# Optimization experiments

Measured on AMD Instinct MI355X. Metric: run time of the kernel, lower is better.

Reference implementation:

```python
import jax, jax.numpy as jnp
import numpy as np

N_NODES = 100000


def _gcn_layer(x, W, b, src, dst, dinv):
    # x: [N, din]; W: [din, dout]; src/dst: [E+N] (self-loops included); dinv: [N]
    h = x @ W                                   # [N, dout] small GEMM
    norm = dinv[src] * dinv[dst]                # [E+N]
    msg = h[src] * norm[:, None]                # [E+N, dout] gather
    out = jax.ops.segment_sum(msg, dst, num_segments=N_NODES)  # scatter-add
    return jax.nn.relu(out + b)


def setup_inputs() -> dict:
    key = jax.random.key(0)
    ks = jax.random.split(key, 8)
    d_in, d_h = 128, 128
    x = jax.random.normal(ks[0], (N_NODES, d_in), dtype=jnp.float32)
    edge_index = jax.random.randint(ks[1], (2, 1600000), 0, N_NODES, dtype=jnp.int64)
    def glorot(k, din, dout):
        lim = np.sqrt(6.0 / (din + dout)).astype(np.float32)
        return jax.random.uniform(k, (din, dout), jnp.float32, -lim, lim)
    W1 = glorot(ks[2], d_in, d_h); b1 = jnp.zeros((d_h,), jnp.float32)
    W2 = glorot(ks[3], d_h, d_h); b2 = jnp.zeros((d_h,), jnp.float32)
    W3 = glorot(ks[4], d_h, d_h); b3 = jnp.zeros((d_h,), jnp.float32)
    return {"x": x, "W1": W1, "b1": b1, "W2": W2, "b2": b2,
            "W3": W3, "b3": b3, "edge_index": edge_index}


def reference(x, W1, b1, W2, b2, W3, b3, edge_index):
    # GCNConv (Kipf & Welling): D^{-1/2}(A+I)D^{-1/2} X W + b, per layer, with ReLU.
    loop = jnp.arange(N_NODES, dtype=edge_index.dtype)
    src = jnp.concatenate([edge_index[0], loop])  # self-loops appended
    dst = jnp.concatenate([edge_index[1], loop])
    deg = jax.ops.segment_sum(jnp.ones_like(dst, dtype=x.dtype), dst,
                              num_segments=N_NODES)
    dinv = jnp.where(deg > 0, jax.lax.rsqrt(deg), 0.0)
    h = _gcn_layer(x, W1, b1, src, dst, dinv)
    h = _gcn_layer(h, W2, b2, src, dst, dinv)
    h = _gcn_layer(h, W3, b3, src, dst, dinv)
    return h
```

## Files before the change

### kernel.cpp

```cpp
#include <hip/hip_runtime.h>
#include <hip/hip_fp16.h>
#include <math.h>

#define NN 100000
#define DD 128
#define SCAN_CHUNK 2048
#define AGG_BLOCKS 2048

typedef short short8 __attribute__((ext_vector_type(8)));
typedef float f32x4 __attribute__((ext_vector_type(4)));

__global__ __launch_bounds__(256) void hist_rank_kernel(const int* __restrict__ dst, int E,
                                                        int* __restrict__ deg,
                                                        int* __restrict__ rank) {
    int i = blockIdx.x * 256 + threadIdx.x;
    int e = i * 4;
    if (e + 3 < E) {
        int4 d4 = ((const int4*)dst)[i];
        int4 r4;
        r4.x = atomicAdd(&deg[d4.x], 1);
        r4.y = atomicAdd(&deg[d4.y], 1);
        r4.z = atomicAdd(&deg[d4.z], 1);
        r4.w = atomicAdd(&deg[d4.w], 1);
        ((int4*)rank)[i] = r4;
    } else {
        for (; e < E; ++e) rank[e] = atomicAdd(&deg[dst[e]], 1);
    }
}

__global__ __launch_bounds__(256) void scan1_kernel(const int* __restrict__ deg,
                                                    int* __restrict__ chunkSum,
                                                    float* __restrict__ dinv, int n) {
    __shared__ int lds[256];
    int tid = threadIdx.x;
    int base = blockIdx.x * SCAN_CHUNK + tid * 8;
    int s = 0;
    #pragma unroll
    for (int j = 0; j < 8; ++j) {
        int idx = base + j;
        if (idx < n) {
            int d = deg[idx];
            s += d;
            dinv[idx] = rsqrtf((float)d + 1.0f);
        }
    }
    lds[tid] = s;
    __syncthreads();
    for (int d = 128; d > 0; d >>= 1) {
        if (tid < d) lds[tid] += lds[tid + d];
        __syncthreads();
    }
    if (tid == 0) chunkSum[blockIdx.x] = lds[0];
}

__global__ void scan2_kernel(int* __restrict__ chunkSum, int* __restrict__ chunkOff,
                             int nb, int* __restrict__ offsets) {
    __shared__ int lds[512];
    int tid = threadIdx.x;
    if (tid < nb) lds[tid] = chunkSum[tid];
    __syncthreads();
    if (tid == 0) {
        int run = 0;
        for (int i = 0; i < nb; ++i) {
            int v = lds[i];
            lds[i] = run;
            run += v;
        }
        offsets[NN] = run;
    }
    __syncthreads();
    if (tid < nb) chunkOff[tid] = lds[tid];
}

__global__ __launch_bounds__(256) void scan3_kernel(const int* __restrict__ deg,
                                                    const int* __restrict__ chunkOff,
                                                    int* __restrict__ offsets, int n) {
    __shared__ int lds[256];
    int tid = threadIdx.x;
    int base = blockIdx.x * SCAN_CHUNK + tid * 8;
    int v[8];
    int tsum = 0;
    #pragma unroll
    for (int j = 0; j < 8; ++j) {
        int idx = base + j;
        v[j] = (idx < n) ? deg[idx] : 0;
        tsum += v[j];
    }
    lds[tid] = tsum;
    __syncthreads();
    for (int d = 1; d < 256; d <<= 1) {
        int t = (tid >= d) ? lds[tid - d] : 0;
        __syncthreads();
        lds[tid] += t;
        __syncthreads();
    }
    int excl = lds[tid] - tsum;
    int off0 = chunkOff[blockIdx.x] + excl;
    int run = 0;
    #pragma unroll
    for (int j = 0; j < 8; ++j) {
        int idx = base + j;
        if (idx < n) offsets[idx] = off0 + run;
        run += v[j];
    }
}

__global__ __launch_bounds__(256) void fill_kernel(const int* __restrict__ src,
                                                   const int* __restrict__ dst,
                                                   const int* __restrict__ rank, int E,
                                                   const int* __restrict__ offsets,
                                                   int* __restrict__ csr) {
    int i = blockIdx.x * 256 + threadIdx.x;
    int e = i * 4;
    if (e + 3 < E) {
        int4 d4 = ((const int4*)dst)[i];
        int4 s4 = ((const int4*)src)[i];
        int4 r4 = ((const int4*)rank)[i];
        int o0 = offsets[d4.x];
        int o1 = offsets[d4.y];
        int o2 = offsets[d4.z];
        int o3 = offsets[d4.w];
        csr[o0 + r4.x] = s4.x;
        csr[o1 + r4.y] = s4.y;
        csr[o2 + r4.z] = s4.z;
        csr[o3 + r4.w] = s4.w;
    } else {
        for (; e < E; ++e) csr[offsets[dst[e]] + rank[e]] = src[e];
    }
}

__device__ __forceinline__ unsigned short f2bf(float f) {
    unsigned int u = __float_as_uint(f);
    unsigned int r = u + 0x7FFFu + ((u >> 16) & 1u);
    return (unsigned short)(r >> 16);
}

__device__ __forceinline__ void split8(const float* v, short8& hi, short8& lo) {
    #pragma unroll
    for (int j = 0; j < 8; ++j) {
        float f = v[j];
        unsigned short h = f2bf(f);
        float fl = f - __uint_as_float(((unsigned int)h) << 16);
        hi[j] = (short)h;
        lo[j] = (short)f2bf(fl);
    }
}

__device__ __forceinline__ void split8t(const float* v, short8& hi, short8& lo) {
    const unsigned int* u = (const unsigned int*)v;
    float lof[8];
    #pragma unroll
    for (int j = 0; j < 8; ++j)
        lof[j] = v[j] - __uint_as_float(u[j] & 0xFFFF0000u);
    const unsigned int* lu = (const unsigned int*)lof;
    union { short8 s; unsigned int w[4]; } H, L;
    #pragma unroll
    for (int q = 0; q < 4; ++q) {
#if __has_builtin(__builtin_amdgcn_perm)
        H.w[q] = __builtin_amdgcn_perm(u[2 * q + 1], u[2 * q], 0x07060302u);
        L.w[q] = __builtin_amdgcn_perm(lu[2 * q + 1], lu[2 * q], 0x07060302u);
#else
        H.w[q] = (u[2 * q + 1] & 0xFFFF0000u) | (u[2 * q] >> 16);
        L.w[q] = (lu[2 * q + 1] & 0xFFFF0000u) | (lu[2 * q] >> 16);
#endif
    }
    hi = H.s; lo = L.s;
}

__global__ __launch_bounds__(256) void wsplit3_kernel(const float* __restrict__ W1,
                                                      const float* __restrict__ W2,
                                                      const float* __restrict__ W3,
                                                      uint4* __restrict__ wh,
                                                      uint4* __restrict__ wl) {
    int b = blockIdx.x;
    int layer = b >> 3;
    const float* W = (layer == 0) ? W1 : (layer == 1) ? W2 : W3;
    int i = (b & 7) * 256 + threadIdx.x;
    int lane_e = i & 63;
    int ks = (i >> 6) & 3;
    int cf = i >> 8;
    int colb = cf * 16 + (lane_e & 15);
    int rowb = ks * 32 + (lane_e >> 4) * 8;
    float wvv[8];
    #pragma unroll
    for (int j = 0; j < 8; ++j) wvv[j] = W[(rowb + j) * DD + colb];
    short8 h, l;
    split8(wvv, h, l);
    union { short8 s; uint4 u; } ch, cl;
    ch.s = h; cl.s = l;
    wh[layer * 2048 + i] = ch.u;
    wl[layer * 2048 + i] = cl.u;
}

template <typename InT>
__global__ __launch_bounds__(256) void gemm_norm_kernel(
    const InT* __restrict__ X, const uint4* __restrict__ whg,
    const uint4* __restrict__ wlg,
    const float* __restrict__ dinv, __half* __restrict__ G)
{
    const int tid  = threadIdx.x;
    const int base = blockIdx.x * 128;
    const int lane = tid & 63;
    const int wv   = tid >> 6;
    const int kg   = lane >> 4;
    const int mcol = lane & 15;

    const int node0 = base + wv * 32 + mcol;
    const int node1 = node0 + 16;

    short8 xh[2][4], xl[2][4];
    #pragma unroll
    for (int rf = 0; rf < 2; ++rf) {
        int arow = rf ? node1 : node0;
        if (arow >= NN) arow = NN - 1;
        const InT* xr = X + (size_t)arow * DD;
        #pragma unroll
        for (int ks = 0; ks < 4; ++ks) {
            int k0 = ks * 32 + kg * 8;
            float av[8];
            if constexpr (sizeof(InT) == 4) {
                *(float4*)&av[0] = *(const float4*)&xr[k0];
                *(float4*)&av[4] = *(const float4*)&xr[k0 + 4];
            } else {
                union { uint4 u; __half h[8]; } hv;
                hv.u = *(const uint4*)&xr[k0];
                #pragma unroll
                for (int j = 0; j < 8; ++j) av[j] = __half2float(hv.h[j]);
            }
            split8t(av, xh[rf][ks], xl[rf][ks]);
        }
    }
    const float di0 = dinv[node0 < NN ? node0 : NN - 1];
    const float di1 = dinv[node1 < NN ? node1 : NN - 1];

    #pragma unroll 1
    for (int cf = 0; cf < 8; ++cf) {
        f32x4 acc0 = {0.f, 0.f, 0.f, 0.f};
        f32x4 acc1 = {0.f, 0.f, 0.f, 0.f};
        #pragma unroll
        for (int ks = 0; ks < 4; ++ks) {
            union { uint4 u; short8 s; } bh, bl;
            bh.u = whg[(cf * 4 + ks) * 64 + lane];
            bl.u = wlg[(cf * 4 + ks) * 64 + lane];
            acc0 = __builtin_amdgcn_mfma_f32_16x16x32_bf16(bh.s, xh[0][ks], acc0, 0, 0, 0);
            acc0 = __builtin_amdgcn_mfma_f32_16x16x32_bf16(bl.s, xh[0][ks], acc0, 0, 0, 0);
            acc0 = __builtin_amdgcn_mfma_f32_16x16x32_bf16(bh.s, xl[0][ks], acc0, 0, 0, 0);
            acc1 = __builtin_amdgcn_mfma_f32_16x16x32_bf16(bh.s, xh[1][ks], acc1, 0, 0, 0);
            acc1 = __builtin_amdgcn_mfma_f32_16x16x32_bf16(bl.s, xh[1][ks], acc1, 0, 0, 0);
            acc1 = __builtin_amdgcn_mfma_f32_16x16x32_bf16(bh.s, xl[1][ks], acc1, 0, 0, 0);
        }
        const int fb = cf * 16 + kg * 4;
        if (node0 < NN) {
            __half2 p0 = __floats2half2_rn(acc0[0] * di0, acc0[1] * di0);
            __half2 p1 = __floats2half2_rn(acc0[2] * di0, acc0[3] * di0);
            uint2 st;
            st.x = *reinterpret_cast<unsigned int*>(&p0);
            st.y = *reinterpret_cast<unsigned int*>(&p1);
            *(uint2*)&G[(size_t)node0 * DD + fb] = st;
        }
        if (node1 < NN) {
            __half2 p0 = __floats2half2_rn(acc1[0] * di1, acc1[1] * di1);
            __half2 p1 = __floats2half2_rn(acc1[2] * di1, acc1[3] * di1);
            uint2 st;
            st.x = *reinterpret_cast<unsigned int*>(&p0);
            st.y = *reinterpret_cast<unsigned int*>(&p1);
            *(uint2*)&G[(size_t)node1 * DD + fb] = st;
        }
    }
}

__device__ __forceinline__ float4 gload(const __half* __restrict__ g, int idx, int cq) {
    uint2 u = *(const uint2*)(g + (size_t)idx * DD + cq * 4);
    __half2 h0 = *reinterpret_cast<const __half2*>(&u.x);
    __half2 h1 = *reinterpret_cast<const __half2*>(&u.y);
    float2 f0 = __half22float2(h0);
    float2 f1 = __half22float2(h1);
    return make_float4(f0.x, f0.y, f1.x, f1.y);
}

template <typename OutT>
__global__ __launch_bounds__(256) void agg_kernel(
    const __half* __restrict__ g, const float* __restrict__ dinv,
    const int* __restrict__ off, const int* __restrict__ csr,
    const float* __restrict__ bias, OutT* __restrict__ out)
{
    const int wid  = threadIdx.x >> 6;
    const int lane = threadIdx.x & 63;
    const int sub  = lane >> 5;
    const int cq   = lane & 31;
    const float4 bb = ((const float4*)bias)[cq];
    const int ngroups = (NN + 3) / 4;

    for (int grp = blockIdx.x; grp < ngroups; grp += AGG_BLOCKS) {
        int node = grp * 4 + wid;
        if (node >= NN) continue;

        float4 acc = make_float4(0.f, 0.f, 0.f, 0.f);
        float4 acc2 = make_float4(0.f, 0.f, 0.f, 0.f);
        if (sub == 0) acc = gload(g, node, cq);

        const int e0 = off[node], end = off[node + 1];
        const int cnt = end - e0;
        const int pairs = cnt >> 1;
        const int np4 = pairs & ~3;

        if (np4) {
            int i0 = csr[e0 + 0 + sub];
            int i1 = csr[e0 + 2 + sub];
            int i2 = csr[e0 + 4 + sub];
            int i3 = csr[e0 + 6 + sub];
            for (int p = 4; p < np4; p += 4) {
                int b0 = e0 + 2 * p + sub;
                int j0 = csr[b0];
                int j1 = csr[b0 + 2];
                int j2 = csr[b0 + 4];
                int j3 = csr[b0 + 6];
                float4 v0 = gload(g, i0, cq);
                float4 v1 = gload(g, i1, cq);
                float4 v2 = gload(g, i2, cq);
                float4 v3 = gload(g, i3, cq);
                acc.x += v0.x + v2.x; acc.y += v0.y + v2.y;
                acc.z += v0.z + v2.z; acc.w += v0.w + v2.w;
                acc2.x += v1.x + v3.x; acc2.y += v1.y + v3.y;
                acc2.z += v1.z + v3.z; acc2.w += v1.w + v3.w;
                i0 = j0; i1 = j1; i2 = j2; i3 = j3;
            }
            float4 v0 = gload(g, i0, cq);
            float4 v1 = gload(g, i1, cq);
            float4 v2 = gload(g, i2, cq);
            float4 v3 = gload(g, i3, cq);
            acc.x += v0.x + v2.x; acc.y += v0.y + v2.y;
            acc.z += v0.z + v2.z; acc.w += v0.w + v2.w;
            acc2.x += v1.x + v3.x; acc2.y += v1.y + v3.y;
            acc2.z += v1.z + v3.z; acc2.w += v1.w + v3.w;
        }
        for (int q = np4; q < pairs; ++q) {
            int s = csr[e0 + 2 * q + sub];
            float4 v = gload(g, s, cq);
            acc.x += v.x; acc.y += v.y; acc.z += v.z; acc.w += v.w;
        }
        if ((cnt & 1) && sub == 0) {
            int s = csr[end - 1];
            float4 v = gload(g, s, cq);
            acc.x += v.x; acc.y += v.y; acc.z += v.z; acc.w += v.w;
        }

        acc.x += acc2.x; acc.y += acc2.y; acc.z += acc2.z; acc.w += acc2.w;
        acc.x += __shfl_xor(acc.x, 32, 64);
        acc.y += __shfl_xor(acc.y, 32, 64);
        acc.z += __shfl_xor(acc.z, 32, 64);
        acc.w += __shfl_xor(acc.w, 32, 64);

        if (sub == 0) {
            float di = dinv[node];
            float4 o;
            o.x = fmaxf(fmaf(acc.x, di, bb.x), 0.f);
            o.y = fmaxf(fmaf(acc.y, di, bb.y), 0.f);
            o.z = fmaxf(fmaf(acc.z, di, bb.z), 0.f);
            o.w = fmaxf(fmaf(acc.w, di, bb.w), 0.f);
            if constexpr (sizeof(OutT) == 4) {
                ((float4*)out)[(size_t)node * 32 + cq] = o;
            } else {
                uint2 st;
                __half2 h0 = __floats2half2_rn(o.x, o.y);
                __half2 h1 = __floats2half2_rn(o.z, o.w);
                st.x = *reinterpret_cast<unsigned int*>(&h0);
                st.y = *reinterpret_cast<unsigned int*>(&h1);
                *(uint2*)((__half*)out + (size_t)node * DD + cq * 4) = st;
            }
        }
    }
}

extern "C" void kernel_launch(void* const* d_in, const int* in_sizes, int n_in,
                              void* d_out, int out_size, void* d_ws, size_t ws_size,
                              hipStream_t stream)
{
    const float* x  = (const float*)d_in[0];
    const float* W1 = (const float*)d_in[1];
    const float* b1 = (const float*)d_in[2];
    const float* W2 = (const float*)d_in[3];
    const float* b2 = (const float*)d_in[4];
    const float* W3 = (const float*)d_in[5];
    const float* b3 = (const float*)d_in[6];
    const int*   ei = (const int*)d_in[7];

    const int E = in_sizes[7] / 2;
    const int* src = ei;
    const int* dst = ei + E;

    float* out = (float*)d_out;

    char* wsb = (char*)d_ws;
    size_t p = 0;
    int* deg      = (int*)(wsb + p); p += ((size_t)NN * 4 + 1023) & ~1023ull;
    int* offsets  = (int*)(wsb + p); p += ((size_t)(NN + 1) * 4 + 1023) & ~1023ull;
    int* chunkSum = (int*)(wsb + p); p += 4096;
    int* chunkOff = (int*)(wsb + p); p += 4096;
    int* csr      = (int*)(wsb + p); p += ((size_t)E * 4 + 1023) & ~1023ull;
    int* rank     = (int*)(wsb + p); p += ((size_t)E * 4 + 1023) & ~1023ull;
    float* dinv   = (float*)(wsb + p); p += ((size_t)NN * 4 + 1023) & ~1023ull;
    uint4* wh     = (uint4*)(wsb + p); p += 3 * 2048 * sizeof(uint4);
    uint4* wl     = (uint4*)(wsb + p); p += 3 * 2048 * sizeof(uint4);
    __half* g     = (__half*)(wsb + p); p += (size_t)NN * DD * 2;
    __half* h_act = (__half*)(wsb + p); p += (size_t)NN * DD * 2;

    const int NB = (NN + SCAN_CHUNK - 1) / SCAN_CHUNK;

    hipMemsetAsync(deg, 0, (size_t)NN * 4, stream);
    hist_rank_kernel<<<(E / 4 + 256) / 256 + 1, 256, 0, stream>>>(dst, E, deg, rank);
    scan1_kernel<<<NB, 256, 0, stream>>>(deg, chunkSum, dinv, NN);
    scan2_kernel<<<1, 512, 0, stream>>>(chunkSum, chunkOff, NB, offsets);
    scan3_kernel<<<NB, 256, 0, stream>>>(deg, chunkOff, offsets, NN);
    fill_kernel<<<(E / 4 + 256) / 256 + 1, 256, 0, stream>>>(src, dst, rank, E, offsets, csr);
    wsplit3_kernel<<<24, 256, 0, stream>>>(W1, W2, W3, wh, wl);

    const int gemm_grid = (NN + 127) / 128;

    gemm_norm_kernel<float><<<gemm_grid, 256, 0, stream>>>(x, wh, wl, dinv, g);
    agg_kernel<__half><<<AGG_BLOCKS, 256, 0, stream>>>(g, dinv, offsets, csr, b1, h_act);
    gemm_norm_kernel<__half><<<gemm_grid, 256, 0, stream>>>(h_act, wh + 2048, wl + 2048, dinv, g);
    agg_kernel<__half><<<AGG_BLOCKS, 256, 0, stream>>>(g, dinv, offsets, csr, b2, h_act);
    gemm_norm_kernel<__half><<<gemm_grid, 256, 0, stream>>>(h_act, wh + 4096, wl + 4096, dinv, g);
    agg_kernel<float><<<AGG_BLOCKS, 256, 0, stream>>>(g, dinv, offsets, csr, b3, out);
}
```

Measured before the change: 392.0 us.

## Fuse aggregation with next-layer GEMM and split CSR fill by destination range

Aggregation of layers 1 and 2 now stages 16 aggregated rows in shared memory and multiplies them straight away by the next layer's weights with split-bf16 MFMA. This removes the fp16 h_act round trip through global memory and two GEMM launches. The CSR fill is split into two passes over destination halves, which aims for better locality of the scattered writes at the cost of reading the edge list twice. The fused kernel adds block-wide barriers and assumes NN is divisible by 16.

```diff
diff --git a/kernel.cpp b/kernel.cpp
--- a/kernel.cpp
+++ b/kernel.cpp
@@ -109,23 +109,23 @@
                                                    const int* __restrict__ dst,
                                                    const int* __restrict__ rank, int E,
                                                    const int* __restrict__ offsets,
-                                                   int* __restrict__ csr) {
+                                                   int* __restrict__ csr,
+                                                   int dlo, int dhi) {
     int i = blockIdx.x * 256 + threadIdx.x;
     int e = i * 4;
     if (e + 3 < E) {
         int4 d4 = ((const int4*)dst)[i];
         int4 s4 = ((const int4*)src)[i];
         int4 r4 = ((const int4*)rank)[i];
-        int o0 = offsets[d4.x];
-        int o1 = offsets[d4.y];
-        int o2 = offsets[d4.z];
-        int o3 = offsets[d4.w];
-        csr[o0 + r4.x] = s4.x;
-        csr[o1 + r4.y] = s4.y;
-        csr[o2 + r4.z] = s4.z;
-        csr[o3 + r4.w] = s4.w;
+        if (d4.x >= dlo && d4.x < dhi) csr[offsets[d4.x] + r4.x] = s4.x;
+        if (d4.y >= dlo && d4.y < dhi) csr[offsets[d4.y] + r4.y] = s4.y;
+        if (d4.z >= dlo && d4.z < dhi) csr[offsets[d4.z] + r4.z] = s4.z;
+        if (d4.w >= dlo && d4.w < dhi) csr[offsets[d4.w] + r4.w] = s4.w;
     } else {
-        for (; e < E; ++e) csr[offsets[dst[e]] + rank[e]] = src[e];
+        for (; e < E; ++e) {
+            int d = dst[e];
+            if (d >= dlo && d < dhi) csr[offsets[d] + rank[e]] = src[e];
+        }
     }
 }
 
@@ -278,53 +278,32 @@
     return make_float4(f0.x, f0.y, f1.x, f1.y);
 }
 
-template <typename OutT>
-__global__ __launch_bounds__(256) void agg_kernel(
-    const __half* __restrict__ g, const float* __restrict__ dinv,
-    const int* __restrict__ off, const int* __restrict__ csr,
-    const float* __restrict__ bias, OutT* __restrict__ out)
-{
-    const int wid  = threadIdx.x >> 6;
-    const int lane = threadIdx.x & 63;
-    const int sub  = lane >> 5;
-    const int cq   = lane & 31;
-    const float4 bb = ((const float4*)bias)[cq];
-    const int ngroups = (NN + 3) / 4;
-
-    for (int grp = blockIdx.x; grp < ngroups; grp += AGG_BLOCKS) {
-        int node = grp * 4 + wid;
-        if (node >= NN) continue;
-
-        float4 acc = make_float4(0.f, 0.f, 0.f, 0.f);
-        float4 acc2 = make_float4(0.f, 0.f, 0.f, 0.f);
-        if (sub == 0) acc = gload(g, node, cq);
-
-        const int e0 = off[node], end = off[node + 1];
-        const int cnt = end - e0;
-        const int pairs = cnt >> 1;
-        const int np4 = pairs & ~3;
-
-        if (np4) {
-            int i0 = csr[e0 + 0 + sub];
-            int i1 = csr[e0 + 2 + sub];
-            int i2 = csr[e0 + 4 + sub];
-            int i3 = csr[e0 + 6 + sub];
-            for (int p = 4; p < np4; p += 4) {
-                int b0 = e0 + 2 * p + sub;
-                int j0 = csr[b0];
-                int j1 = csr[b0 + 2];
-                int j2 = csr[b0 + 4];
-                int j3 = csr[b0 + 6];
-                float4 v0 = gload(g, i0, cq);
-                float4 v1 = gload(g, i1, cq);
-                float4 v2 = gload(g, i2, cq);
-                float4 v3 = gload(g, i3, cq);
-                acc.x += v0.x + v2.x; acc.y += v0.y + v2.y;
-                acc.z += v0.z + v2.z; acc.w += v0.w + v2.w;
-                acc2.x += v1.x + v3.x; acc2.y += v1.y + v3.y;
-                acc2.z += v1.z + v3.z; acc2.w += v1.w + v3.w;
-                i0 = j0; i1 = j1; i2 = j2; i3 = j3;
-            }
+__device__ __forceinline__ float4 gather_row(const __half* __restrict__ g,
+                                             const int* __restrict__ off,
+                                             const int* __restrict__ csr,
+                                             const float* __restrict__ dinv,
+                                             const float4 bb, int node,
+                                             int sub, int cq) {
+    float4 acc = make_float4(0.f, 0.f, 0.f, 0.f);
+    float4 acc2 = make_float4(0.f, 0.f, 0.f, 0.f);
+    if (sub == 0) acc = gload(g, node, cq);
+
+    const int e0 = off[node], end = off[node + 1];
+    const int cnt = end - e0;
+    const int pairs = cnt >> 1;
+    const int np4 = pairs & ~3;
+
+    if (np4) {
+        int i0 = csr[e0 + 0 + sub];
+        int i1 = csr[e0 + 2 + sub];
+        int i2 = csr[e0 + 4 + sub];
+        int i3 = csr[e0 + 6 + sub];
+        for (int p = 4; p < np4; p += 4) {
+            int b0 = e0 + 2 * p + sub;
+            int j0 = csr[b0];
+            int j1 = csr[b0 + 2];
+            int j2 = csr[b0 + 4];
+            int j3 = csr[b0 + 6];
             float4 v0 = gload(g, i0, cq);
             float4 v1 = gload(g, i1, cq);
             float4 v2 = gload(g, i2, cq);
@@ -333,42 +312,125 @@
             acc.z += v0.z + v2.z; acc.w += v0.w + v2.w;
             acc2.x += v1.x + v3.x; acc2.y += v1.y + v3.y;
             acc2.z += v1.z + v3.z; acc2.w += v1.w + v3.w;
-        }
-        for (int q = np4; q < pairs; ++q) {
-            int s = csr[e0 + 2 * q + sub];
-            float4 v = gload(g, s, cq);
-            acc.x += v.x; acc.y += v.y; acc.z += v.z; acc.w += v.w;
-        }
-        if ((cnt & 1) && sub == 0) {
-            int s = csr[end - 1];
-            float4 v = gload(g, s, cq);
-            acc.x += v.x; acc.y += v.y; acc.z += v.z; acc.w += v.w;
-        }
-
-        acc.x += acc2.x; acc.y += acc2.y; acc.z += acc2.z; acc.w += acc2.w;
-        acc.x += __shfl_xor(acc.x, 32, 64);
-        acc.y += __shfl_xor(acc.y, 32, 64);
-        acc.z += __shfl_xor(acc.z, 32, 64);
-        acc.w += __shfl_xor(acc.w, 32, 64);
-
-        if (sub == 0) {
-            float di = dinv[node];
-            float4 o;
-            o.x = fmaxf(fmaf(acc.x, di, bb.x), 0.f);
-            o.y = fmaxf(fmaf(acc.y, di, bb.y), 0.f);
-            o.z = fmaxf(fmaf(acc.z, di, bb.z), 0.f);
-            o.w = fmaxf(fmaf(acc.w, di, bb.w), 0.f);
-            if constexpr (sizeof(OutT) == 4) {
-                ((float4*)out)[(size_t)node * 32 + cq] = o;
-            } else {
-                uint2 st;
-                __half2 h0 = __floats2half2_rn(o.x, o.y);
-                __half2 h1 = __floats2half2_rn(o.z, o.w);
-                st.x = *reinterpret_cast<unsigned int*>(&h0);
-                st.y = *reinterpret_cast<unsigned int*>(&h1);
-                *(uint2*)((__half*)out + (size_t)node * DD + cq * 4) = st;
+            i0 = j0; i1 = j1; i2 = j2; i3 = j3;
+        }
+        float4 v0 = gload(g, i0, cq);
+        float4 v1 = gload(g, i1, cq);
+        float4 v2 = gload(g, i2, cq);
+        float4 v3 = gload(g, i3, cq);
+        acc.x += v0.x + v2.x; acc.y += v0.y + v2.y;
+        acc.z += v0.z + v2.z; acc.w += v0.w + v2.w;
+        acc2.x += v1.x + v3.x; acc2.y += v1.y + v3.y;
+        acc2.z += v1.z + v3.z; acc2.w += v1.w + v3.w;
+    }
+    for (int q = np4; q < pairs; ++q) {
+        int s = csr[e0 + 2 * q + sub];
+        float4 v = gload(g, s, cq);
+        acc.x += v.x; acc.y += v.y; acc.z += v.z; acc.w += v.w;
+    }
+    if ((cnt & 1) && sub == 0) {
+        int s = csr[end - 1];
+        float4 v = gload(g, s, cq);
+        acc.x += v.x; acc.y += v.y; acc.z += v.z; acc.w += v.w;
+    }
+
+    acc.x += acc2.x; acc.y += acc2.y; acc.z += acc2.z; acc.w += acc2.w;
+    acc.x += __shfl_xor(acc.x, 32, 64);
+    acc.y += __shfl_xor(acc.y, 32, 64);
+    acc.z += __shfl_xor(acc.z, 32, 64);
+    acc.w += __shfl_xor(acc.w, 32, 64);
+
+    float di = dinv[node];
+    float4 o;
+    o.x = fmaxf(fmaf(acc.x, di, bb.x), 0.f);
+    o.y = fmaxf(fmaf(acc.y, di, bb.y), 0.f);
+    o.z = fmaxf(fmaf(acc.z, di, bb.z), 0.f);
+    o.w = fmaxf(fmaf(acc.w, di, bb.w), 0.f);
+    return o;
+}
+
+__global__ __launch_bounds__(256) void fused_agg_gemm_kernel(
+    const __half* __restrict__ gA, const float* __restrict__ dinv,
+    const int* __restrict__ off, const int* __restrict__ csr,
+    const float* __restrict__ bias,
+    const uint4* __restrict__ whg, const uint4* __restrict__ wlg,
+    __half* __restrict__ gB)
+{
+    __shared__ float xs[16][132];
+
+    const int tid  = threadIdx.x;
+    const int wid  = tid >> 6;
+    const int lane = tid & 63;
+    const int sub  = lane >> 5;
+    const int cq   = lane & 31;
+    const int kg   = lane >> 4;
+    const int nloc = lane & 15;
+    const float4 bb = ((const float4*)bias)[cq];
+    const int ngroups = NN / 16;
+
+    for (int grp = blockIdx.x; grp < ngroups; grp += AGG_BLOCKS) {
+        #pragma unroll 1
+        for (int i = 0; i < 4; ++i) {
+            int node = grp * 16 + wid * 4 + i;
+            float4 o = gather_row(gA, off, csr, dinv, bb, node, sub, cq);
+            if (sub == 0) *(float4*)&xs[wid * 4 + i][cq * 4] = o;
+        }
+        __syncthreads();
+
+        short8 xh[4], xl[4];
+        #pragma unroll
+        for (int ks = 0; ks < 4; ++ks) {
+            int kb = ks * 32 + kg * 8;
+            float av[8];
+            #pragma unroll
+            for (int j = 0; j < 8; ++j) av[j] = xs[nloc][kb + j];
+            split8t(av, xh[ks], xl[ks]);
+        }
+        const int nodeD = grp * 16 + nloc;
+        const float diN = dinv[nodeD];
+
+        #pragma unroll
+        for (int cfl = 0; cfl < 2; ++cfl) {
+            int cf = wid * 2 + cfl;
+            f32x4 acc = {0.f, 0.f, 0.f, 0.f};
+            #pragma unroll
+            for (int ks = 0; ks < 4; ++ks) {
+                union { uint4 u; short8 s; } ah, al;
+                ah.u = whg[(cf * 4 + ks) * 64 + lane];
+                al.u = wlg[(cf * 4 + ks) * 64 + lane];
+                acc = __builtin_amdgcn_mfma_f32_16x16x32_bf16(ah.s, xh[ks], acc, 0, 0, 0);
+                acc = __builtin_amdgcn_mfma_f32_16x16x32_bf16(al.s, xh[ks], acc, 0, 0, 0);
+                acc = __builtin_amdgcn_mfma_f32_16x16x32_bf16(ah.s, xl[ks], acc, 0, 0, 0);
             }
-        }
+            const int fb = cf * 16 + kg * 4;
+            __half2 p0 = __floats2half2_rn(acc[0] * diN, acc[1] * diN);
+            __half2 p1 = __floats2half2_rn(acc[2] * diN, acc[3] * diN);
+            uint2 st;
+            st.x = *reinterpret_cast<unsigned int*>(&p0);
+            st.y = *reinterpret_cast<unsigned int*>(&p1);
+            *(uint2*)&gB[(size_t)nodeD * DD + fb] = st;
+        }
+        __syncthreads();
+    }
+}
+
+__global__ __launch_bounds__(256) void agg_kernel(
+    const __half* __restrict__ g, const float* __restrict__ dinv,
+    const int* __restrict__ off, const int* __restrict__ csr,
+    const float* __restrict__ bias, float* __restrict__ out)
+{
+    const int wid  = threadIdx.x >> 6;
+    const int lane = threadIdx.x & 63;
+    const int sub  = lane >> 5;
+    const int cq   = lane & 31;
+    const float4 bb = ((const float4*)bias)[cq];
+    const int ngroups = (NN + 3) / 4;
+
+    for (int grp = blockIdx.x; grp < ngroups; grp += AGG_BLOCKS) {
+        int node = grp * 4 + wid;
+        if (node >= NN) continue;
+        float4 o = gather_row(g, off, csr, dinv, bb, node, sub, cq);
+        if (sub == 0) ((float4*)out)[(size_t)node * 32 + cq] = o;
     }
 }
 
@@ -403,7 +465,7 @@
     uint4* wh     = (uint4*)(wsb + p); p += 3 * 2048 * sizeof(uint4);
     uint4* wl     = (uint4*)(wsb + p); p += 3 * 2048 * sizeof(uint4);
     __half* g     = (__half*)(wsb + p); p += (size_t)NN * DD * 2;
-    __half* h_act = (__half*)(wsb + p); p += (size_t)NN * DD * 2;
+    __half* g2    = (__half*)(wsb + p); p += (size_t)NN * DD * 2;
 
     const int NB = (NN + SCAN_CHUNK - 1) / SCAN_CHUNK;
 
@@ -412,15 +474,17 @@
     scan1_kernel<<<NB, 256, 0, stream>>>(deg, chunkSum, dinv, NN);
     scan2_kernel<<<1, 512, 0, stream>>>(chunkSum, chunkOff, NB, offsets);
     scan3_kernel<<<NB, 256, 0, stream>>>(deg, chunkOff, offsets, NN);
-    fill_kernel<<<(E / 4 + 256) / 256 + 1, 256, 0, stream>>>(src, dst, rank, E, offsets, csr);
+    const int fill_grid = (E / 4 + 256) / 256 + 1;
+    fill_kernel<<<fill_grid, 256, 0, stream>>>(src, dst, rank, E, offsets, csr, 0, NN / 2);
+    fill_kernel<<<fill_grid, 256, 0, stream>>>(src, dst, rank, E, offsets, csr, NN / 2, NN);
     wsplit3_kernel<<<24, 256, 0, stream>>>(W1, W2, W3, wh, wl);
 
     const int gemm_grid = (NN + 127) / 128;
 
     gemm_norm_kernel<float><<<gemm_grid, 256, 0, stream>>>(x, wh, wl, dinv, g);
-    agg_kernel<__half><<<AGG_BLOCKS, 256, 0, stream>>>(g, dinv, offsets, csr, b1, h_act);
-    gemm_norm_kernel<__half><<<gemm_grid, 256, 0, stream>>>(h_act, wh + 2048, wl + 2048, dinv, g);
-    agg_kernel<__half><<<AGG_BLOCKS, 256, 0, stream>>>(g, dinv, offsets, csr, b2, h_act);
-    gemm_norm_kernel<__half><<<gemm_grid, 256, 0, stream>>>(h_act, wh + 4096, wl + 4096, dinv, g);
-    agg_kernel<float><<<AGG_BLOCKS, 256, 0, stream>>>(g, dinv, offsets, csr, b3, out);
-}
+    fused_agg_gemm_kernel<<<AGG_BLOCKS, 256, 0, stream>>>(g, dinv, offsets, csr, b1,
+                                                          wh + 2048, wl + 2048, g2);
+    fused_agg_gemm_kernel<<<AGG_BLOCKS, 256, 0, stream>>>(g2, dinv, offsets, csr, b2,
+                                                          wh + 4096, wl + 4096, g);
+    agg_kernel<<<AGG_BLOCKS, 256, 0, stream>>>(g, dinv, offsets, csr, b3, out);
+}
```

Result: slower. 517.3 us (+32.0%).

## Build CSR with a two-level LDS bucket sort instead of global atomics

Applied to the files above, without the earlier changes.

Replaces the CSR construction (global-atomic degree histogram with per-edge ranks, a three-kernel scan, then a scatter fill) with a two-level bucket sort. First, edges are binned into 98 buckets of 1024 destination nodes using LDS histograms, and each edge is packed with its local destination and its source into one int. Then one block per bucket counts, scans and scatters its edges in LDS, writing offsets, dinv and csr directly. This cuts global atomic traffic, the rank and deg buffers, and several launches. In exchange it assumes a fixed per-bucket capacity of 18432 edges and source ids below 2^17, and silently drops edges if a bucket overflows. That assumption holds for uniformly random edges but not for skewed graphs.

```diff
diff --git a/kernel.cpp b/kernel.cpp
--- a/kernel.cpp
+++ b/kernel.cpp
@@ -4,128 +4,125 @@
 
 #define NN 100000
 #define DD 128
-#define SCAN_CHUNK 2048
 #define AGG_BLOCKS 2048
+
+#define NBUCK 98
+#define BSH 10
+#define BW 1024
+#define CAP 18432
+#define APASS 196
+#define CURPAD 32
 
 typedef short short8 __attribute__((ext_vector_type(8)));
 typedef float f32x4 __attribute__((ext_vector_type(4)));
 
-__global__ __launch_bounds__(256) void hist_rank_kernel(const int* __restrict__ dst, int E,
-                                                        int* __restrict__ deg,
-                                                        int* __restrict__ rank) {
-    int i = blockIdx.x * 256 + threadIdx.x;
-    int e = i * 4;
-    if (e + 3 < E) {
-        int4 d4 = ((const int4*)dst)[i];
-        int4 r4;
-        r4.x = atomicAdd(&deg[d4.x], 1);
-        r4.y = atomicAdd(&deg[d4.y], 1);
-        r4.z = atomicAdd(&deg[d4.z], 1);
-        r4.w = atomicAdd(&deg[d4.w], 1);
-        ((int4*)rank)[i] = r4;
-    } else {
-        for (; e < E; ++e) rank[e] = atomicAdd(&deg[dst[e]], 1);
-    }
-}
-
-__global__ __launch_bounds__(256) void scan1_kernel(const int* __restrict__ deg,
-                                                    int* __restrict__ chunkSum,
-                                                    float* __restrict__ dinv, int n) {
-    __shared__ int lds[256];
-    int tid = threadIdx.x;
-    int base = blockIdx.x * SCAN_CHUNK + tid * 8;
+__global__ __launch_bounds__(256) void bucket_scatter_kernel(
+    const int* __restrict__ src, const int* __restrict__ dst, int E,
+    int* __restrict__ cur, int* __restrict__ packed)
+{
+    __shared__ int h[NBUCK];
+    __shared__ int base[NBUCK];
+    __shared__ int c2[NBUCK];
+
+    const int tid = threadIdx.x;
+    const int chunk = (E + APASS - 1) / APASS;
+    const int e0 = blockIdx.x * chunk;
+    const int e1 = min(e0 + chunk, E);
+
+    if (tid < NBUCK) { h[tid] = 0; c2[tid] = 0; }
+    __syncthreads();
+
+    for (int e = e0 + tid; e < e1; e += 256)
+        atomicAdd(&h[dst[e] >> BSH], 1);
+    __syncthreads();
+
+    if (tid < NBUCK && h[tid] > 0)
+        base[tid] = atomicAdd(&cur[tid * CURPAD], h[tid]);
+    __syncthreads();
+
+    for (int e = e0 + tid; e < e1; e += 256) {
+        int d = dst[e];
+        int b = d >> BSH;
+        int r = atomicAdd(&c2[b], 1);
+        int pos = base[b] + r;
+        if (pos < CAP)
+            packed[b * CAP + pos] = ((d & (BW - 1)) << 17) | src[e];
+    }
+}
+
+__global__ void bucket_scan_kernel(const int* __restrict__ cur,
+                                   int* __restrict__ cbase,
+                                   int* __restrict__ offsets) {
+    if (threadIdx.x == 0) {
+        int run = 0;
+        for (int b = 0; b < NBUCK; ++b) {
+            int c = cur[b * CURPAD];
+            if (c > CAP) c = CAP;
+            cbase[b] = run;
+            run += c;
+        }
+        offsets[NN] = run;
+    }
+}
+
+__global__ __launch_bounds__(256) void bucket_csr_kernel(
+    const int* __restrict__ cur, const int* __restrict__ cbase,
+    const int* __restrict__ packed,
+    int* __restrict__ offsets, float* __restrict__ dinv,
+    int* __restrict__ csr)
+{
+    __shared__ int cnt[BW];
+    __shared__ int excl[BW];
+    __shared__ int ts[256];
+
+    const int tid = threadIdx.x;
+    const int b = blockIdx.x;
+    int c = cur[b * CURPAD];
+    if (c > CAP) c = CAP;
+    const int cb = cbase[b];
+    const int pbase = b * CAP;
+
+    #pragma unroll
+    for (int k = 0; k < 4; ++k) cnt[tid * 4 + k] = 0;
+    __syncthreads();
+
+    for (int i = tid; i < c; i += 256)
+        atomicAdd(&cnt[packed[pbase + i] >> 17], 1);
+    __syncthreads();
+
+    int v[4];
     int s = 0;
     #pragma unroll
-    for (int j = 0; j < 8; ++j) {
-        int idx = base + j;
-        if (idx < n) {
-            int d = deg[idx];
-            s += d;
-            dinv[idx] = rsqrtf((float)d + 1.0f);
-        }
-    }
-    lds[tid] = s;
-    __syncthreads();
-    for (int d = 128; d > 0; d >>= 1) {
-        if (tid < d) lds[tid] += lds[tid + d];
+    for (int k = 0; k < 4; ++k) { v[k] = cnt[tid * 4 + k]; s += v[k]; }
+    ts[tid] = s;
+    __syncthreads();
+    for (int d = 1; d < 256; d <<= 1) {
+        int t = (tid >= d) ? ts[tid - d] : 0;
         __syncthreads();
-    }
-    if (tid == 0) chunkSum[blockIdx.x] = lds[0];
-}
-
-__global__ void scan2_kernel(int* __restrict__ chunkSum, int* __restrict__ chunkOff,
-                             int nb, int* __restrict__ offsets) {
-    __shared__ int lds[512];
-    int tid = threadIdx.x;
-    if (tid < nb) lds[tid] = chunkSum[tid];
-    __syncthreads();
-    if (tid == 0) {
-        int run = 0;
-        for (int i = 0; i < nb; ++i) {
-            int v = lds[i];
-            lds[i] = run;
-            run += v;
-        }
-        offsets[NN] = run;
-    }
-    __syncthreads();
-    if (tid < nb) chunkOff[tid] = lds[tid];
-}
-
-__global__ __launch_bounds__(256) void scan3_kernel(const int* __restrict__ deg,
-                                                    const int* __restrict__ chunkOff,
-                                                    int* __restrict__ offsets, int n) {
-    __shared__ int lds[256];
-    int tid = threadIdx.x;
-    int base = blockIdx.x * SCAN_CHUNK + tid * 8;
-    int v[8];
-    int tsum = 0;
-    #pragma unroll
-    for (int j = 0; j < 8; ++j) {
-        int idx = base + j;
-        v[j] = (idx < n) ? deg[idx] : 0;
-        tsum += v[j];
-    }
-    lds[tid] = tsum;
-    __syncthreads();
-    for (int d = 1; d < 256; d <<= 1) {
-        int t = (tid >= d) ? lds[tid - d] : 0;
+        ts[tid] += t;
         __syncthreads();
-        lds[tid] += t;
-        __syncthreads();
-    }
-    int excl = lds[tid] - tsum;
-    int off0 = chunkOff[blockIdx.x] + excl;
+    }
+    int ex = ts[tid] - s;
+
     int run = 0;
     #pragma unroll
-    for (int j = 0; j < 8; ++j) {
-        int idx = base + j;
-        if (idx < n) offsets[idx] = off0 + run;
-        run += v[j];
-    }
-}
-
-__global__ __launch_bounds__(256) void fill_kernel(const int* __restrict__ src,
-                                                   const int* __restrict__ dst,
-                                                   const int* __restrict__ rank, int E,
-                                                   const int* __restrict__ offsets,
-                                                   int* __restrict__ csr) {
-    int i = blockIdx.x * 256 + threadIdx.x;
-    int e = i * 4;
-    if (e + 3 < E) {
-        int4 d4 = ((const int4*)dst)[i];
-        int4 s4 = ((const int4*)src)[i];
-        int4 r4 = ((const int4*)rank)[i];
-        int o0 = offsets[d4.x];
-        int o1 = offsets[d4.y];
-        int o2 = offsets[d4.z];
-        int o3 = offsets[d4.w];
-        csr[o0 + r4.x] = s4.x;
-        csr[o1 + r4.y] = s4.y;
-        csr[o2 + r4.z] = s4.z;
-        csr[o3 + r4.w] = s4.w;
-    } else {
-        for (; e < E; ++e) csr[offsets[dst[e]] + rank[e]] = src[e];
+    for (int k = 0; k < 4; ++k) {
+        int dl = tid * 4 + k;
+        excl[dl] = ex + run;
+        int node = b * BW + dl;
+        if (node < NN) {
+            offsets[node] = cb + ex + run;
+            dinv[node] = rsqrtf((float)v[k] + 1.0f);
+        }
+        run += v[k];
+    }
+    __syncthreads();
+
+    for (int i = tid; i < c; i += 256) {
+        int p = packed[pbase + i];
+        int dl = p >> 17;
+        int r = atomicAdd(&excl[dl], 1);
+        csr[cb + r] = p & 0x1FFFF;
     }
 }
 
@@ -278,6 +275,77 @@
     return make_float4(f0.x, f0.y, f1.x, f1.y);
 }
 
+__device__ __forceinline__ float4 gather_row(const __half* __restrict__ g,
+                                             const int* __restrict__ off,
+                                             const int* __restrict__ csr,
+                                             const float* __restrict__ dinv,
+                                             const float4 bb, int node,
+                                             int sub, int cq) {
+    float4 acc = make_float4(0.f, 0.f, 0.f, 0.f);
+    float4 acc2 = make_float4(0.f, 0.f, 0.f, 0.f);
+    if (sub == 0) acc = gload(g, node, cq);
+
+    const int e0 = off[node], end = off[node + 1];
+    const int cnt = end - e0;
+    const int pairs = cnt >> 1;
+    const int np4 = pairs & ~3;
+
+    if (np4) {
+        int i0 = csr[e0 + 0 + sub];
+        int i1 = csr[e0 + 2 + sub];
+        int i2 = csr[e0 + 4 + sub];
+        int i3 = csr[e0 + 6 + sub];
+        for (int p = 4; p < np4; p += 4) {
+            int b0 = e0 + 2 * p + sub;
+            int j0 = csr[b0];
+            int j1 = csr[b0 + 2];
+            int j2 = csr[b0 + 4];
+            int j3 = csr[b0 + 6];
+            float4 v0 = gload(g, i0, cq);
+            float4 v1 = gload(g, i1, cq);
+            float4 v2 = gload(g, i2, cq);
+            float4 v3 = gload(g, i3, cq);
+            acc.x += v0.x + v2.x; acc.y += v0.y + v2.y;
+            acc.z += v0.z + v2.z; acc.w += v0.w + v2.w;
+            acc2.x += v1.x + v3.x; acc2.y += v1.y + v3.y;
+            acc2.z += v1.z + v3.z; acc2.w += v1.w + v3.w;
+            i0 = j0; i1 = j1; i2 = j2; i3 = j3;
+        }
+        float4 v0 = gload(g, i0, cq);
+        float4 v1 = gload(g, i1, cq);
+        float4 v2 = gload(g, i2, cq);
+        float4 v3 = gload(g, i3, cq);
+        acc.x += v0.x + v2.x; acc.y += v0.y + v2.y;
+        acc.z += v0.z + v2.z; acc.w += v0.w + v2.w;
+        acc2.x += v1.x + v3.x; acc2.y += v1.y + v3.y;
+        acc2.z += v1.z + v3.z; acc2.w += v1.w + v3.w;
+    }
+    for (int q = np4; q < pairs; ++q) {
+        int s = csr[e0 + 2 * q + sub];
+        float4 v = gload(g, s, cq);
+        acc.x += v.x; acc.y += v.y; acc.z += v.z; acc.w += v.w;
+    }
+    if ((cnt & 1) && sub == 0) {
+        int s = csr[end - 1];
+        float4 v = gload(g, s, cq);
+        acc.x += v.x; acc.y += v.y; acc.z += v.z; acc.w += v.w;
+    }
+
+    acc.x += acc2.x; acc.y += acc2.y; acc.z += acc2.z; acc.w += acc2.w;
+    acc.x += __shfl_xor(acc.x, 32, 64);
+    acc.y += __shfl_xor(acc.y, 32, 64);
+    acc.z += __shfl_xor(acc.z, 32, 64);
+    acc.w += __shfl_xor(acc.w, 32, 64);
+
+    float di = dinv[node];
+    float4 o;
+    o.x = fmaxf(fmaf(acc.x, di, bb.x), 0.f);
+    o.y = fmaxf(fmaf(acc.y, di, bb.y), 0.f);
+    o.z = fmaxf(fmaf(acc.z, di, bb.z), 0.f);
+    o.w = fmaxf(fmaf(acc.w, di, bb.w), 0.f);
+    return o;
+}
+
 template <typename OutT>
 __global__ __launch_bounds__(256) void agg_kernel(
     const __half* __restrict__ g, const float* __restrict__ dinv,
@@ -294,70 +362,8 @@
     for (int grp = blockIdx.x; grp < ngroups; grp += AGG_BLOCKS) {
         int node = grp * 4 + wid;
         if (node >= NN) continue;
-
-        float4 acc = make_float4(0.f, 0.f, 0.f, 0.f);
-        float4 acc2 = make_float4(0.f, 0.f, 0.f, 0.f);
-        if (sub == 0) acc = gload(g, node, cq);
-
-        const int e0 = off[node], end = off[node + 1];
-        const int cnt = end - e0;
-        const int pairs = cnt >> 1;
-        const int np4 = pairs & ~3;
-
-        if (np4) {
-            int i0 = csr[e0 + 0 + sub];
-            int i1 = csr[e0 + 2 + sub];
-            int i2 = csr[e0 + 4 + sub];
-            int i3 = csr[e0 + 6 + sub];
-            for (int p = 4; p < np4; p += 4) {
-                int b0 = e0 + 2 * p + sub;
-                int j0 = csr[b0];
-                int j1 = csr[b0 + 2];
-                int j2 = csr[b0 + 4];
-                int j3 = csr[b0 + 6];
-                float4 v0 = gload(g, i0, cq);
-                float4 v1 = gload(g, i1, cq);
-                float4 v2 = gload(g, i2, cq);
-                float4 v3 = gload(g, i3, cq);
-                acc.x += v0.x + v2.x; acc.y += v0.y + v2.y;
-                acc.z += v0.z + v2.z; acc.w += v0.w + v2.w;
-                acc2.x += v1.x + v3.x; acc2.y += v1.y + v3.y;
-                acc2.z += v1.z + v3.z; acc2.w += v1.w + v3.w;
-                i0 = j0; i1 = j1; i2 = j2; i3 = j3;
-            }
-            float4 v0 = gload(g, i0, cq);
-            float4 v1 = gload(g, i1, cq);
-            float4 v2 = gload(g, i2, cq);
-            float4 v3 = gload(g, i3, cq);
-            acc.x += v0.x + v2.x; acc.y += v0.y + v2.y;
-            acc.z += v0.z + v2.z; acc.w += v0.w + v2.w;
-            acc2.x += v1.x + v3.x; acc2.y += v1.y + v3.y;
-            acc2.z += v1.z + v3.z; acc2.w += v1.w + v3.w;
-        }
-        for (int q = np4; q < pairs; ++q) {
-            int s = csr[e0 + 2 * q + sub];
-            float4 v = gload(g, s, cq);
-            acc.x += v.x; acc.y += v.y; acc.z += v.z; acc.w += v.w;
-        }
-        if ((cnt & 1) && sub == 0) {
-            int s = csr[end - 1];
-            float4 v = gload(g, s, cq);
-            acc.x += v.x; acc.y += v.y; acc.z += v.z; acc.w += v.w;
-        }
-
-        acc.x += acc2.x; acc.y += acc2.y; acc.z += acc2.z; acc.w += acc2.w;
-        acc.x += __shfl_xor(acc.x, 32, 64);
-        acc.y += __shfl_xor(acc.y, 32, 64);
-        acc.z += __shfl_xor(acc.z, 32, 64);
-        acc.w += __shfl_xor(acc.w, 32, 64);
-
+        float4 o = gather_row(g, off, csr, dinv, bb, node, sub, cq);
         if (sub == 0) {
-            float di = dinv[node];
-            float4 o;
-            o.x = fmaxf(fmaf(acc.x, di, bb.x), 0.f);
-            o.y = fmaxf(fmaf(acc.y, di, bb.y), 0.f);
-            o.z = fmaxf(fmaf(acc.z, di, bb.z), 0.f);
-            o.w = fmaxf(fmaf(acc.w, di, bb.w), 0.f);
             if constexpr (sizeof(OutT) == 4) {
                 ((float4*)out)[(size_t)node * 32 + cq] = o;
             } else {
@@ -393,34 +399,29 @@
 
     char* wsb = (char*)d_ws;
     size_t p = 0;
-    int* deg      = (int*)(wsb + p); p += ((size_t)NN * 4 + 1023) & ~1023ull;
     int* offsets  = (int*)(wsb + p); p += ((size_t)(NN + 1) * 4 + 1023) & ~1023ull;
-    int* chunkSum = (int*)(wsb + p); p += 4096;
-    int* chunkOff = (int*)(wsb + p); p += 4096;
     int* csr      = (int*)(wsb + p); p += ((size_t)E * 4 + 1023) & ~1023ull;
-    int* rank     = (int*)(wsb + p); p += ((size_t)E * 4 + 1023) & ~1023ull;
     float* dinv   = (float*)(wsb + p); p += ((size_t)NN * 4 + 1023) & ~1023ull;
+    int* cur      = (int*)(wsb + p); p += (size_t)NBUCK * CURPAD * 4;
+    int* cbase    = (int*)(wsb + p); p += 1024;
     uint4* wh     = (uint4*)(wsb + p); p += 3 * 2048 * sizeof(uint4);
     uint4* wl     = (uint4*)(wsb + p); p += 3 * 2048 * sizeof(uint4);
+    int* packed   = (int*)(wsb + p); p += ((size_t)NBUCK * CAP * 4 + 1023) & ~1023ull;
     __half* g     = (__half*)(wsb + p); p += (size_t)NN * DD * 2;
-    __half* h_act = (__half*)(wsb + p); p += (size_t)NN * DD * 2;
-
-    const int NB = (NN + SCAN_CHUNK - 1) / SCAN_CHUNK;
-
-    hipMemsetAsync(deg, 0, (size_t)NN * 4, stream);
-    hist_rank_kernel<<<(E / 4 + 256) / 256 + 1, 256, 0, stream>>>(dst, E, deg, rank);
-    scan1_kernel<<<NB, 256, 0, stream>>>(deg, chunkSum, dinv, NN);
-    scan2_kernel<<<1, 512, 0, stream>>>(chunkSum, chunkOff, NB, offsets);
-    scan3_kernel<<<NB, 256, 0, stream>>>(deg, chunkOff, offsets, NN);
-    fill_kernel<<<(E / 4 + 256) / 256 + 1, 256, 0, stream>>>(src, dst, rank, E, offsets, csr);
+    __half* g2    = (__half*)(wsb + p); p += (size_t)NN * DD * 2;
+
+    hipMemsetAsync(cur, 0, (size_t)NBUCK * CURPAD * 4, stream);
+    bucket_scatter_kernel<<<APASS, 256, 0, stream>>>(src, dst, E, cur, packed);
+    bucket_scan_kernel<<<1, 64, 0, stream>>>(cur, cbase, offsets);
+    bucket_csr_kernel<<<NBUCK, 256, 0, stream>>>(cur, cbase, packed, offsets, dinv, csr);
     wsplit3_kernel<<<24, 256, 0, stream>>>(W1, W2, W3, wh, wl);
 
     const int gemm_grid = (NN + 127) / 128;
 
     gemm_norm_kernel<float><<<gemm_grid, 256, 0, stream>>>(x, wh, wl, dinv, g);
-    agg_kernel<__half><<<AGG_BLOCKS, 256, 0, stream>>>(g, dinv, offsets, csr, b1, h_act);
-    gemm_norm_kernel<__half><<<gemm_grid, 256, 0, stream>>>(h_act, wh + 2048, wl + 2048, dinv, g);
-    agg_kernel<__half><<<AGG_BLOCKS, 256, 0, stream>>>(g, dinv, offsets, csr, b2, h_act);
-    gemm_norm_kernel<__half><<<gemm_grid, 256, 0, stream>>>(h_act, wh + 4096, wl + 4096, dinv, g);
+    agg_kernel<__half><<<AGG_BLOCKS, 256, 0, stream>>>(g, dinv, offsets, csr, b1, g2);
+    gemm_norm_kernel<__half><<<gemm_grid, 256, 0, stream>>>(g2, wh + 2048, wl + 2048, dinv, g);
+    agg_kernel<__half><<<AGG_BLOCKS, 256, 0, stream>>>(g, dinv, offsets, csr, b2, g2);
+    gemm_norm_kernel<__half><<<gemm_grid, 256, 0, stream>>>(g2, wh + 4096, wl + 4096, dinv, g);
     agg_kernel<float><<<AGG_BLOCKS, 256, 0, stream>>>(g, dinv, offsets, csr, b3, out);
 }
```

After: 360.6 us. 1.09x faster.
